# Kernel tuning notes

Measured on AMD Instinct MI355X. Metric: run time of the kernel, lower is better.

Reference implementation:

```python
import jax, jax.numpy as jnp
import numpy as np

SR = 48000.0


def _lin_interp(x, n):
    # Matches torch F.interpolate(mode='linear', align_corners=False) on last axis.
    T = x.shape[-1]
    pos = (jnp.arange(n, dtype=jnp.float32) + 0.5) * (T / n) - 0.5
    pos = jnp.clip(pos, 0.0, T - 1)
    i0 = jnp.floor(pos).astype(jnp.int32)
    i1 = jnp.minimum(i0 + 1, T - 1)
    w = (pos - i0.astype(jnp.float32)).astype(x.dtype)
    return jnp.take(x, i0, axis=-1) * (1.0 - w) + jnp.take(x, i1, axis=-1) * w


def setup_inputs() -> dict:
    key = jax.random.key(0)
    k1, k2, k3 = jax.random.split(key, 3)
    B, T, N = 16, 250, 100
    harm_amps = jax.random.uniform(k1, (B, T, N), dtype=jnp.float32)
    # realistic fundamental frequencies: 80..480 Hz
    f0_hz = 80.0 + 400.0 * jax.random.uniform(k2, (B, T), dtype=jnp.float32)
    # small inharmonicity coefficients (piano-like): ~0..1e-4
    inh = 1e-4 * jax.random.uniform(k3, (B,), dtype=jnp.float32)
    return {"harm_amps": harm_amps, "f0_hz": f0_hz, "inh": inh, "n_samples": 48000}


def reference(harm_amps, f0_hz, inh, n_samples):
    B, T, N = harm_amps.shape
    # upsample amplitudes (B,N,n_samples) and f0 (B,n_samples)
    a = _lin_interp(jnp.transpose(harm_amps, (0, 2, 1)), n_samples)
    f0_up = _lin_interp(f0_hz, n_samples)
    k = jnp.arange(1, N + 1, dtype=jnp.float32)  # harmonic numbers 1..N
    stretch = jnp.sqrt(1.0 + inh[:, None] * k ** 2)  # (B,N)
    inst_freq = f0_up[:, None, :] * (k[None, :] * stretch)[:, :, None]  # (B,N,n)
    nyq_mask = (inst_freq < SR * 0.45).astype(a.dtype)
    phase = jnp.cumsum(2.0 * jnp.pi * inst_freq / SR, axis=-1)
    signal = jnp.sum(a * nyq_mask * jnp.sin(phase), axis=1, keepdims=True)  # (B,1,n)
    return signal / N
```

## Files before the change

kernel.cpp:

```cpp
#include <hip/hip_runtime.h>
#include <cmath>

#pragma clang fp contract(off)

#define SRF   48000.0f
#define NYQF  21600.0f
constexpr float  TWO_PI_F  = 6.283185307179586476925286766559f;
constexpr double INV_2PI_D = 0.15915494309189533576888376337251;
constexpr float  RC1 = (float)INV_2PI_D;
constexpr float  RC2 = (float)(INV_2PI_D - (double)RC1);
constexpr double INV_SR_D = 1.0 / 48000.0;
constexpr float  DD1 = (float)INV_SR_D;
constexpr float  DD2 = (float)(INV_SR_D - (double)DD1);

__device__ __forceinline__ float hsin_rev(float r) {
#if __has_builtin(__builtin_amdgcn_sinf)
    return __builtin_amdgcn_sinf(r);
#else
    return __sinf(r * TWO_PI_F);
#endif
}

__device__ __forceinline__ float div48000(float t) {
    float h = t * DD1;
    float r = __builtin_fmaf(t, DD1, -h);
    float s = __builtin_fmaf(t, DD2, r);
    return h + s;
}

__device__ __forceinline__ float sin_phase(float ph) {
    float h  = ph * RC1;
    float r  = __builtin_fmaf(ph, RC1, -h);
    float s  = __builtin_fmaf(ph, RC2, r);
    float nn = __builtin_rintf(h);
    float fr = (h - nn) + s;
    return hsin_rev(fr);
}

template <int IDX>
__device__ __forceinline__ float grp4_bcast(float v, int lb) {
#if __has_builtin(__builtin_amdgcn_ds_swizzle)
    constexpr int imm = (IDX << 5) | 0x1C;
    return __int_as_float(__builtin_amdgcn_ds_swizzle(__float_as_int(v), imm));
#else
    return __shfl(v, lb + IDX);
#endif
}

__device__ __forceinline__ float kcval(int k, float ib) {
    float kf = (float)(k + 1);
    float k2 = kf * kf;
    float m  = ib * k2;
    float s1 = 1.0f + m;
    float st = (float)sqrt((double)s1);
    return kf * st;
}

__global__ void __launch_bounds__(256) k_f0up(const float* __restrict__ f0,
        float* __restrict__ f0up, float* __restrict__ out,
        int T, int n, float pf) {
    int j = blockIdx.x * 256 + threadIdx.x;
    int b = blockIdx.y;
    if (j >= n) return;
    float pos = ((float)j + 0.5f);
    pos = pos * pf;
    pos = pos - 0.5f;
    pos = fmaxf(pos, 0.0f);
    pos = fminf(pos, (float)(T - 1));
    int   i0 = (int)pos;
    int   i1 = min(i0 + 1, T - 1);
    float w  = pos - (float)i0;
    float omw = 1.0f - w;
    const float* fb = f0 + b * T;
    f0up[(size_t)b * n + j] = fb[i0] * omw + fb[i1] * w;
    out[(size_t)b * n + j]  = 0.0f;
}

__global__ void __launch_bounds__(256) k_scan4(const float* __restrict__ f0up,
        const float* __restrict__ inh, float* __restrict__ scan4,
        int N, int n) {
    __shared__ float lv[6016];
    const int k   = blockIdx.x;
    const int b   = blockIdx.y;
    const int tid = threadIdx.x;
    const float kc = kcval(k, inh[b]);
    const float4* f4 = (const float4*)(f0up + (size_t)b * n);
    const int len4 = n >> 4;

    auto l2of = [&](float4 v) -> float {
        float a0 = div48000(TWO_PI_F * (kc * v.x));
        float a1 = div48000(TWO_PI_F * (kc * v.y));
        float a2 = div48000(TWO_PI_F * (kc * v.z));
        float a3 = div48000(TWO_PI_F * (kc * v.w));
        return (a0 + a1) + (a2 + a3);
    };
    for (int i = tid; i < len4; i += 256) {
        float s01 = l2of(f4[4*i])     + l2of(f4[4*i + 1]);
        float s23 = l2of(f4[4*i + 2]) + l2of(f4[4*i + 3]);
        lv[i] = s01 + s23;
    }
    __syncthreads();

    int offp = 0, lenp = len4, P = 4;
    for (int l = 5; ; ++l) {
        int lenc = lenp >> 1;
        int offc = offp + lenp;
        for (int i = tid; i < lenc; i += 256)
            lv[offc + i] = lv[offp + 2*i] + lv[offp + 2*i + 1];
        __syncthreads();
        P = l;
        if (lenc == 1) break;
        offp = offc; lenp = lenc;
    }
    for (int l = P - 1; l >= 4; --l) {
        int lenl = n >> l;
        int offl = 0;
        for (int m = 4; m < l; ++m) offl += (n >> m);
        int offh = offl + lenl;
        int lenh = n >> (l + 1);
        float*       arr = lv + offl;
        const float* hi  = lv + offh;
        for (int i = tid; i < lenh; i += 256) {
            float v = hi[i];
            int e = 2*i + 2;
            if (e < lenl) arr[e] = v + arr[e];
            arr[2*i + 1] = v;
        }
        __syncthreads();
    }
    float* sp = scan4 + (size_t)(b * N + k) * (len4 + 1);
    if (tid == 0) sp[0] = 0.0f;
    for (int i = tid; i < len4; i += 256) sp[1 + i] = lv[i];
}

__global__ void __launch_bounds__(256) k_synth4(
        const float* __restrict__ harm, const float* __restrict__ f0up,
        const float* __restrict__ inh,  const float* __restrict__ scan4,
        float* __restrict__ out, int B, int T, int N, int n, float pf, int kpg) {
    const int tid  = threadIdx.x;
    const int b    = blockIdx.y;
    const int k0   = blockIdx.z * kpg;
    const int g    = blockIdx.x * 256 + tid;
    const int q    = g >> 2;
    const int c    = g & 3;
    const int NG   = n >> 4;
    const int NGP  = NG + 1;
    const int kend = min(k0 + kpg, N);
    const int kact = kend - k0;
    const bool valid = q < NG;

    __shared__ float2 amps[8 * 32];
    __shared__ float  kcs[32];

    const float ib    = inh[b];
    const float tmaxf = (float)(T - 1);
    for (int i = tid; i < kact; i += 256) kcs[i] = kcval(k0 + i, ib);

    const int j0blk = blockIdx.x * 1024;
    int i0min;
    {
        float p = ((float)j0blk + 0.5f);
        p = p * pf; p = p - 0.5f;
        p = fmaxf(p, 0.0f); p = fminf(p, tmaxf);
        i0min = (int)p;
    }
    for (int idx = tid; idx < 8 * kact; idx += 256) {
        int r = idx / kact, kk = idx - r * kact;
        int r0 = min(i0min + r, T - 1);
        int r1 = min(i0min + r + 1, T - 1);
        float a0 = harm[((size_t)b * T + r0) * N + (k0 + kk)];
        float a1 = harm[((size_t)b * T + r1) * N + (k0 + kk)];
        amps[idx] = make_float2(a0, a1 - a0);
    }
    __syncthreads();

    float u0=0.f,u1=0.f,u2=0.f,u3=0.f;
    float w0=0.f,w1=0.f,w2=0.f,w3=0.f;
    int   a0o=0,a1o=0,a2o=0,a3o=0;
    float um = __builtin_inff();
    if (valid) {
        const float4 v = *(const float4*)(f0up + (size_t)b * n + (size_t)q * 16 + c * 4);
        u0=v.x; u1=v.y; u2=v.z; u3=v.w;
        um = fminf(fminf(u0,u1), fminf(u2,u3));
        const int jb = q * 16 + c * 4;
        #pragma unroll
        for (int i = 0; i < 4; ++i) {
            float p = ((float)(jb + i) + 0.5f);
            p = p * pf; p = p - 0.5f;
            p = fmaxf(p, 0.0f); p = fminf(p, tmaxf);
            int i0 = (int)p;
            float wv = p - (float)i0;
            int aoo  = (i0 - i0min) * kact;
            if (i==0){w0=wv;a0o=aoo;}
            else if (i==1){w1=wv;a1o=aoo;}
            else if (i==2){w2=wv;a2o=aoo;}
            else {w3=wv;a3o=aoo;}
        }
    }
    #pragma unroll
    for (int off = 32; off > 0; off >>= 1)
        um = fminf(um, __shfl_xor(um, off));
    const float umin = um;
    const int lb = (tid & 63) & ~3;

    if (valid) {
        float acc0=0.f, acc1=0.f, acc2=0.f, acc3=0.f;
        const float* s4k = scan4 + (size_t)(b * N + k0) * NGP;
        float g0c = s4k[q];
        float g1c = s4k[q + 1];

        for (int k = k0; k < kend; ++k) {
            const int   kk = k - k0;
            const float kc = kcs[kk];
            if (kc * umin >= NYQF) break;
            const float G0 = g0c, G1 = g1c;
            if (k + 1 < kend) {
                const float* nx = s4k + NGP;
                g0c = nx[q];
                g1c = nx[q + 1];
                s4k = nx;
            }

            float x0 = div48000(TWO_PI_F * (kc * u0));
            float x1 = div48000(TWO_PI_F * (kc * u1));
            float x2 = div48000(TWO_PI_F * (kc * u2));
            float x3 = div48000(TWO_PI_F * (kc * u3));
            float L1p = x0 + x1, L1q = x2 + x3;
            float L2  = L1p + L1q;

            float s0 = grp4_bcast<0>(L2, lb);
            float s1 = grp4_bcast<1>(L2, lb);
            float s2 = grp4_bcast<2>(L2, lb);
            float t01 = s0 + s1;
            float b1v = G0 + s0;
            float b2v = G0 + t01;
            float b3v = b2v + s2;
            float base = (c == 0) ? G0  : (c == 1) ? b1v : (c == 2) ? b2v : b3v;
            float bn   = (c == 0) ? b1v : (c == 1) ? b2v : (c == 2) ? b3v : G1;

            float ph0 = base + x0;
            float ph1 = base + L1p;
            float ph2 = ph1 + x2;
            float ph3 = bn;

            {   float t1 = kc * u0;
                if (t1 < NYQF) { float sv = sin_phase(ph0);
                    float2 a = amps[a0o + kk];
                    acc0 = __builtin_fmaf(__builtin_fmaf(w0, a.y, a.x), sv, acc0); } }
            {   float t1 = kc * u1;
                if (t1 < NYQF) { float sv = sin_phase(ph1);
                    float2 a = amps[a1o + kk];
                    acc1 = __builtin_fmaf(__builtin_fmaf(w1, a.y, a.x), sv, acc1); } }
            {   float t1 = kc * u2;
                if (t1 < NYQF) { float sv = sin_phase(ph2);
                    float2 a = amps[a2o + kk];
                    acc2 = __builtin_fmaf(__builtin_fmaf(w2, a.y, a.x), sv, acc2); } }
            {   float t1 = kc * u3;
                if (t1 < NYQF) { float sv = sin_phase(ph3);
                    float2 a = amps[a3o + kk];
                    acc3 = __builtin_fmaf(__builtin_fmaf(w3, a.y, a.x), sv, acc3); } }
        }

        const float Nf = (float)N;
        float* ob = out + (size_t)b * n + (size_t)q * 16 + c * 4;
        atomicAdd(&ob[0], acc0 / Nf);
        atomicAdd(&ob[1], acc1 / Nf);
        atomicAdd(&ob[2], acc2 / Nf);
        atomicAdd(&ob[3], acc3 / Nf);
    }
}

__global__ void __launch_bounds__(256) k_scan_synth(
        const float* __restrict__ harm, const float* __restrict__ f0up,
        const float* __restrict__ inh,  float* __restrict__ out,
        int B, int T, int N, int n, float pf) {
    extern __shared__ float lv[];
    const int k   = blockIdx.x;
    const int b   = blockIdx.y;
    const int tid = threadIdx.x;
    const float kc = kcval(k, inh[b]);
    const float* fb = f0up + (size_t)b * n;

    auto inc = [&](int j) -> float {
        float u    = fb[j];
        float inst = kc * u;
        float tt   = TWO_PI_F * inst;
        return tt / SRF;
    };

    const int len1 = n >> 1;
    {
        const float4* f4 = (const float4*)fb;
        for (int i = tid; i < (n >> 2); i += 256) {
            float4 u = f4[i];
            float a0 = (TWO_PI_F * (kc * u.x)) / SRF;
            float a1 = (TWO_PI_F * (kc * u.y)) / SRF;
            float a2 = (TWO_PI_F * (kc * u.z)) / SRF;
            float a3 = (TWO_PI_F * (kc * u.w)) / SRF;
            lv[i] = (a0 + a1) + (a2 + a3);
        }
    }
    __syncthreads();
    int offp = 0, lenp = n >> 2, P = 2;
    for (int l = 3; ; ++l) {
        int lenc = lenp >> 1;
        int offc = offp + lenp;
        for (int i = tid; i < lenc; i += 256)
            lv[offc + i] = lv[offp + 2*i] + lv[offp + 2*i + 1];
        __syncthreads();
        P = l;
        if (lenc == 1) break;
        offp = offc; lenp = lenc;
    }
    for (int l = P - 1; l >= 2; --l) {
        int lenl = n >> l;
        int offl = 0;
        for (int m = 2; m < l; ++m) offl += (n >> m);
        float*       arr = lv + offl;
        const float* hi  = lv + offl + lenl;
        int lenh = n >> (l + 1);
        for (int i = tid; i < lenh; i += 256) {
            float v = hi[i];
            int e = 2*i + 2;
            if (e < lenl) arr[e] = v + arr[e];
            arr[2*i + 1] = v;
        }
        __syncthreads();
    }
    const float* scan2 = lv;

    const float  tmaxf = (float)(T - 1);
    const float  invN  = 1.0f / (float)N;
    const float* hb    = harm + (size_t)b * T * N + k;
    float*       ob    = out + (size_t)b * n;

    auto emit = [&](int j, float ph) {
        float u    = fb[j];
        float inst = kc * u;
        if (!(inst < NYQF)) return;
        double pr = (double)ph * INV_2PI_D;
        double fr = pr - rint(pr);
        float  sv = hsin_rev((float)fr);
        float pos = ((float)j + 0.5f);
        pos = pos * pf; pos = pos - 0.5f;
        pos = fmaxf(pos, 0.0f); pos = fminf(pos, tmaxf);
        int   i0 = (int)pos;
        int   i1 = min(i0 + 1, T - 1);
        float w  = pos - (float)i0;
        float a  = hb[(size_t)i0 * N] * (1.0f - w) + hb[(size_t)i1 * N] * w;
        atomicAdd(&ob[j], (a * sv) * invN);
    };

    if (tid == 0) emit(0, inc(0));
    for (int tt = tid; tt < len1; tt += 256) {
        float s1;
        if (tt == 0)      s1 = inc(0) + inc(1);
        else if (tt & 1)  s1 = scan2[(tt - 1) >> 1];
        else              s1 = scan2[(tt >> 1) - 1] + (inc(2*tt) + inc(2*tt + 1));
        emit(2*tt + 1, s1);
        int je = 2*tt + 2;
        if (je < n) emit(je, s1 + inc(je));
    }
}

extern "C" void kernel_launch(void* const* d_in, const int* in_sizes, int n_in,
                              void* d_out, int out_size, void* d_ws, size_t ws_size,
                              hipStream_t stream) {
    const int B = in_sizes[2];
    const int T = in_sizes[1] / B;
    const int N = in_sizes[0] / (B * T);
    const int n = out_size / B;
    const float pf = (float)((double)T / (double)n);

    const float* harm = (const float*)d_in[0];
    const float* f0   = (const float*)d_in[1];
    const float* inh  = (const float*)d_in[2];
    float* out  = (float*)d_out;
    float* f0up = (float*)d_ws;

    const int KZ  = 4;
    const int kpg = (N + KZ - 1) / KZ;
    const int NG  = n / 16;
    const size_t needFast = (size_t)B * n * 4 + (size_t)B * N * (NG + 1) * 4;
    const bool fast = (ws_size >= needFast) && (n % 16 == 0) && (kpg <= 32);

    k_f0up<<<dim3((n + 255) / 256, B), 256, 0, stream>>>(f0, f0up, out, T, n, pf);

    if (fast) {
        float* scan4 = (float*)((char*)d_ws + (size_t)B * n * 4);
        k_scan4<<<dim3(N, B), 256, 0, stream>>>(f0up, inh, scan4, N, n);
        const int tiles = (NG * 4 + 255) / 256;
        k_synth4<<<dim3(tiles, B, KZ), 256, 0, stream>>>(
            harm, f0up, inh, scan4, out, B, T, N, n, pf, kpg);
    } else {
        const size_t lds_bytes = (size_t)(n / 2) * sizeof(float);
        k_scan_synth<<<dim3(N, B), 256, lds_bytes, stream>>>(
            harm, f0up, inh, out, B, T, N, n, pf);
    }
}
```

Measured before the change: 153.5 us.

## Fuse f0 upsampling into scan and synth kernels, halve harmonic groups

Drops the separate f0 upsampling kernel. The raw f0 row is staged in shared memory, and the scan and synth kernels each interpolate inline. Zeroing of the output is moved into the scan kernel, split across the harmonic blocks. KZ is reduced from 4 to 2, so each synth block handles up to 64 harmonics with larger shared arrays. This removes one launch and the f0up global round-trip, at the cost of recomputing the interpolation and having fewer synth blocks in the grid.

```diff
diff --git a/kernel.cpp b/kernel.cpp
--- a/kernel.cpp
+++ b/kernel.cpp
@@ -54,6 +54,20 @@
     float s1 = 1.0f + m;
     float st = (float)sqrt((double)s1);
     return kf * st;
+}
+
+__device__ __forceinline__ float interp_u(const float* f0s, int j, int T,
+                                          float pf, float tmaxf) {
+    float pos = ((float)j + 0.5f);
+    pos = pos * pf;
+    pos = pos - 0.5f;
+    pos = fmaxf(pos, 0.0f);
+    pos = fminf(pos, tmaxf);
+    int   i0 = (int)pos;
+    int   i1 = min(i0 + 1, T - 1);
+    float w  = pos - (float)i0;
+    float omw = 1.0f - w;
+    return f0s[i0] * omw + f0s[i1] * w;
 }
 
 __global__ void __launch_bounds__(256) k_f0up(const float* __restrict__ f0,
@@ -76,27 +90,37 @@
     out[(size_t)b * n + j]  = 0.0f;
 }
 
-__global__ void __launch_bounds__(256) k_scan4(const float* __restrict__ f0up,
+__global__ void __launch_bounds__(256) k_scan4f(const float* __restrict__ f0,
         const float* __restrict__ inh, float* __restrict__ scan4,
-        int N, int n) {
+        float* __restrict__ out, int N, int T, int n, float pf) {
+    __shared__ float f0s[256];
     __shared__ float lv[6016];
     const int k   = blockIdx.x;
     const int b   = blockIdx.y;
     const int tid = threadIdx.x;
     const float kc = kcval(k, inh[b]);
-    const float4* f4 = (const float4*)(f0up + (size_t)b * n);
+    const float tmaxf = (float)(T - 1);
     const int len4 = n >> 4;
 
-    auto l2of = [&](float4 v) -> float {
-        float a0 = div48000(TWO_PI_F * (kc * v.x));
-        float a1 = div48000(TWO_PI_F * (kc * v.y));
-        float a2 = div48000(TWO_PI_F * (kc * v.z));
-        float a3 = div48000(TWO_PI_F * (kc * v.w));
+    {
+        int chunk = (n + N - 1) / N;
+        int j0 = k * chunk, j1 = min(j0 + chunk, n);
+        for (int j = j0 + tid; j < j1; j += 256) out[(size_t)b * n + j] = 0.0f;
+    }
+    if (tid < T) f0s[tid] = f0[b * T + tid];
+    __syncthreads();
+
+    auto l2of4 = [&](int jb) -> float {
+        float a0 = div48000(TWO_PI_F * (kc * interp_u(f0s, jb,     T, pf, tmaxf)));
+        float a1 = div48000(TWO_PI_F * (kc * interp_u(f0s, jb + 1, T, pf, tmaxf)));
+        float a2 = div48000(TWO_PI_F * (kc * interp_u(f0s, jb + 2, T, pf, tmaxf)));
+        float a3 = div48000(TWO_PI_F * (kc * interp_u(f0s, jb + 3, T, pf, tmaxf)));
         return (a0 + a1) + (a2 + a3);
     };
     for (int i = tid; i < len4; i += 256) {
-        float s01 = l2of(f4[4*i])     + l2of(f4[4*i + 1]);
-        float s23 = l2of(f4[4*i + 2]) + l2of(f4[4*i + 3]);
+        int jb = i * 16;
+        float s01 = l2of4(jb)     + l2of4(jb + 4);
+        float s23 = l2of4(jb + 8) + l2of4(jb + 12);
         lv[i] = s01 + s23;
     }
     __syncthreads();
@@ -133,8 +157,8 @@
     for (int i = tid; i < len4; i += 256) sp[1 + i] = lv[i];
 }
 
-__global__ void __launch_bounds__(256) k_synth4(
-        const float* __restrict__ harm, const float* __restrict__ f0up,
+__global__ void __launch_bounds__(256) k_synth4f(
+        const float* __restrict__ harm, const float* __restrict__ f0,
         const float* __restrict__ inh,  const float* __restrict__ scan4,
         float* __restrict__ out, int B, int T, int N, int n, float pf, int kpg) {
     const int tid  = threadIdx.x;
@@ -149,11 +173,13 @@
     const int kact = kend - k0;
     const bool valid = q < NG;
 
-    __shared__ float2 amps[8 * 32];
-    __shared__ float  kcs[32];
+    __shared__ float2 amps[8 * 64];
+    __shared__ float  kcs[64];
+    __shared__ float  f0s[256];
 
     const float ib    = inh[b];
     const float tmaxf = (float)(T - 1);
+    if (tid < T) f0s[tid] = f0[b * T + tid];
     for (int i = tid; i < kact; i += 256) kcs[i] = kcval(k0 + i, ib);
 
     const int j0blk = blockIdx.x * 1024;
@@ -179,9 +205,6 @@
     int   a0o=0,a1o=0,a2o=0,a3o=0;
     float um = __builtin_inff();
     if (valid) {
-        const float4 v = *(const float4*)(f0up + (size_t)b * n + (size_t)q * 16 + c * 4);
-        u0=v.x; u1=v.y; u2=v.z; u3=v.w;
-        um = fminf(fminf(u0,u1), fminf(u2,u3));
         const int jb = q * 16 + c * 4;
         #pragma unroll
         for (int i = 0; i < 4; ++i) {
@@ -189,13 +212,16 @@
             p = p * pf; p = p - 0.5f;
             p = fmaxf(p, 0.0f); p = fminf(p, tmaxf);
             int i0 = (int)p;
+            int i1 = min(i0 + 1, T - 1);
             float wv = p - (float)i0;
+            float uv = f0s[i0] * (1.0f - wv) + f0s[i1] * wv;
             int aoo  = (i0 - i0min) * kact;
-            if (i==0){w0=wv;a0o=aoo;}
-            else if (i==1){w1=wv;a1o=aoo;}
-            else if (i==2){w2=wv;a2o=aoo;}
-            else {w3=wv;a3o=aoo;}
+            if (i==0){u0=uv;w0=wv;a0o=aoo;}
+            else if (i==1){u1=uv;w1=wv;a1o=aoo;}
+            else if (i==2){u2=uv;w2=wv;a2o=aoo;}
+            else {u3=uv;w3=wv;a3o=aoo;}
         }
+        um = fminf(fminf(u0,u1), fminf(u2,u3));
     }
     #pragma unroll
     for (int off = 32; off > 0; off >>= 1)
@@ -375,24 +401,24 @@
     const float* harm = (const float*)d_in[0];
     const float* f0   = (const float*)d_in[1];
     const float* inh  = (const float*)d_in[2];
-    float* out  = (float*)d_out;
-    float* f0up = (float*)d_ws;
-
-    const int KZ  = 4;
+    float* out = (float*)d_out;
+
+    const int KZ  = 2;
     const int kpg = (N + KZ - 1) / KZ;
     const int NG  = n / 16;
-    const size_t needFast = (size_t)B * n * 4 + (size_t)B * N * (NG + 1) * 4;
-    const bool fast = (ws_size >= needFast) && (n % 16 == 0) && (kpg <= 32);
-
-    k_f0up<<<dim3((n + 255) / 256, B), 256, 0, stream>>>(f0, f0up, out, T, n, pf);
+    const size_t needFast = (size_t)B * N * (NG + 1) * 4;
+    const bool fast = (ws_size >= needFast) && (n % 16 == 0) && (kpg <= 64)
+                      && (T <= 256) && (n >= 16 * N);
 
     if (fast) {
-        float* scan4 = (float*)((char*)d_ws + (size_t)B * n * 4);
-        k_scan4<<<dim3(N, B), 256, 0, stream>>>(f0up, inh, scan4, N, n);
+        float* scan4 = (float*)d_ws;
+        k_scan4f<<<dim3(N, B), 256, 0, stream>>>(f0, inh, scan4, out, N, T, n, pf);
         const int tiles = (NG * 4 + 255) / 256;
-        k_synth4<<<dim3(tiles, B, KZ), 256, 0, stream>>>(
-            harm, f0up, inh, scan4, out, B, T, N, n, pf, kpg);
+        k_synth4f<<<dim3(tiles, B, KZ), 256, 0, stream>>>(
+            harm, f0, inh, scan4, out, B, T, N, n, pf, kpg);
     } else {
+        float* f0up = (float*)d_ws;
+        k_f0up<<<dim3((n + 255) / 256, B), 256, 0, stream>>>(f0, f0up, out, T, n, pf);
         const size_t lds_bytes = (size_t)(n / 2) * sizeof(float);
         k_scan_synth<<<dim3(N, B), 256, lds_bytes, stream>>>(
             harm, f0up, inh, out, B, T, N, n, pf);
```

Result: slower. 171.5 us (+11.7%).
